# Performance work log

Hardware: AMD Instinct MI355X
Metric: run time of the kernel (lower is better)

## Reference

```python
import jax, jax.numpy as jnp
import numpy as np

B, T, D, H = 2, 1024, 1024, 16
K = D            # key_dim = hidden * expand_k (1.0)
V = 2 * D        # value_dim = hidden * expand_v (2.0)
DK, DV = K // H, V // H
I = 2816         # SwiGLU intermediate
CONV = 4
EPS = 1e-6


def rmsnorm(x, w, eps=EPS):
    return x * jax.lax.rsqrt(jnp.mean(x * x, -1, keepdims=True) + eps) * w


def l2norm(x, eps=EPS):
    return x * jax.lax.rsqrt(jnp.sum(x * x, -1, keepdims=True) + eps)


def short_conv(x, w):
    # depthwise causal conv1d (kernel CONV, no bias) + silu; x [B,T,C], w [C,CONV]
    kern = w.T[:, None, :]  # [CONV, 1, C]
    y = jax.lax.conv_general_dilated(
        x, kern, (1,), [(CONV - 1, 0)],
        dimension_numbers=('NWC', 'WIO', 'NWC'),
        feature_group_count=x.shape[-1])
    return jax.nn.silu(y)


def setup_inputs() -> dict:
    key = jax.random.key(0)
    ks = jax.random.split(key, 20)
    p = lambda i, shape, s=0.02: jax.random.normal(ks[i], shape, jnp.float32) * s
    return dict(
        x=jax.random.normal(ks[0], (B, T, D), jnp.float32),
        norm1_w=jnp.ones((D,), jnp.float32),
        wq=p(1, (D, K)), wk=p(2, (D, K)), wv=p(3, (D, V)),
        conv_q=p(4, (K, CONV), 0.3), conv_k=p(5, (K, CONV), 0.3), conv_v=p(6, (V, CONV), 0.3),
        wb=p(7, (D, H)), wa=p(8, (D, H)),
        A_log=jnp.log(jax.random.uniform(ks[9], (H,), jnp.float32, 1.0, 16.0)),
        dt_bias=jnp.log(jnp.expm1(jax.random.uniform(ks[10], (H,), jnp.float32, 0.001, 0.1))),
        wg=p(11, (D, V)),
        o_norm_w=jnp.ones((DV,), jnp.float32),
        wo=p(12, (V, D)),
        norm2_w=jnp.ones((D,), jnp.float32),
        w1=p(13, (D, I)), w2=p(14, (I, D)), w3=p(15, (D, I)),
    )


def reference(x, norm1_w, wq, wk, wv, conv_q, conv_k, conv_v, wb, wa,
              A_log, dt_bias, wg, o_norm_w, wo, norm2_w, w1, w2, w3):
    h = rmsnorm(x, norm1_w)
    # projections + short causal conv (silu)
    q = short_conv(h @ wq, conv_q).reshape(B, T, H, DK)
    k = short_conv(h @ wk, conv_k).reshape(B, T, H, DK)
    v = short_conv(h @ wv, conv_v).reshape(B, T, H, DV)
    q = l2norm(q) * (DK ** -0.5)
    k = l2norm(k)
    beta = jax.nn.sigmoid(h @ wb)                              # [B,T,H]
    # mamba-style decay gate: g = -exp(A_log) * softplus(a + dt_bias)
    g = -jnp.exp(A_log) * jax.nn.softplus(h @ wa + dt_bias)   # [B,T,H]

    # gated delta rule: S_t = exp(g_t)*S_{t-1}; u_t = beta_t*(v_t - k_t^T S_t);
    # S_t += k_t u_t^T; o_t = q_t^T S_t
    def step(S, inp):
        qt, kt, vt, gt, bt = inp                               # [B,H,*]
        S = S * jnp.exp(gt)[..., None, None]
        u = (vt - jnp.einsum('bhk,bhkv->bhv', kt, S)) * bt[..., None]
        S = S + kt[..., None] * u[:, :, None, :]
        ot = jnp.einsum('bhk,bhkv->bhv', qt, S)
        return S, ot

    S0 = jnp.zeros((B, H, DK, DV), x.dtype)
    seq = (q.transpose(1, 0, 2, 3), k.transpose(1, 0, 2, 3),
           v.transpose(1, 0, 2, 3), g.transpose(1, 0, 2), beta.transpose(1, 0, 2))
    _, o = jax.lax.scan(step, S0, seq)
    o = o.transpose(1, 0, 2, 3)                                # [B,T,H,DV]

    # output gate: per-head RMSNorm * swish(gate), then out-projection
    gate = (h @ wg).reshape(B, T, H, DV)
    o = rmsnorm(o, o_norm_w) * gate * jax.nn.sigmoid(gate)
    x = x + o.reshape(B, T, V) @ wo

    # SwiGLU MLP with residual
    h2 = rmsnorm(x, norm2_w)
    return x + (jax.nn.silu(h2 @ w1) * (h2 @ w3)) @ w2
```

## Files before the change

kernel.cpp:

```cpp
#include <hip/hip_runtime.h>
#include <stdint.h>

typedef unsigned short u16;
typedef float f32x4 __attribute__((ext_vector_type(4)));
typedef __bf16 bf16x8 __attribute__((ext_vector_type(8)));
typedef unsigned short u16x8 __attribute__((ext_vector_type(8)));

#define N1P 6272

__device__ __forceinline__ u16 f2bf(float f) {
    union { float f; uint32_t u; } v; v.f = f;
    uint32_t u = v.u;
    return (u16)((u + 0x7FFFu + ((u >> 16) & 1u)) >> 16);
}
__device__ __forceinline__ float bf2f(u16 h) {
    union { uint32_t u; float f; } v; v.u = ((uint32_t)h) << 16; return v.f;
}
__device__ __forceinline__ float sigm(float x) { return 1.f / (1.f + __expf(-x)); }

__device__ __forceinline__ void async16(const u16* g, u16* l) {
    __builtin_amdgcn_global_load_lds((const __attribute__((address_space(1))) void*)g,
                                     (__attribute__((address_space(3))) void*)l, 16, 0, 0);
}

__device__ __forceinline__ int swz64(int row, int col) {
    return row * 128 + ((((col >> 3) ^ (row & 7)) << 3) + (col & 7)) * 2;
}
__device__ __forceinline__ bf16x8 frag64(const u16* m, int rowbase, int lane, int kk) {
    const int row = rowbase + (lane & 15);
    const int unit = (lane >> 4) + (kk << 2);
    return *(const bf16x8*)((const char*)m + row * 128 + ((unit ^ (row & 7)) << 4));
}

struct TJob { const float* src; u16* dst; int rows, cols, rowOff, rowStride, nOut, blkBase, gx; };
struct TJobs { TJob j[10]; };

__global__ __launch_bounds__(256) void k_transpose_all(TJobs jobs, int njobs) {
    __shared__ float tile[32][33];
    const int bid = blockIdx.x;
    int ji = 0;
#pragma unroll
    for (int i = 1; i < 10; ++i)
        if (i < njobs && bid >= jobs.j[i].blkBase) ji = i;
    const TJob J = jobs.j[ji];
    const int bx = bid - J.blkBase;
    const int n0 = (bx % J.gx) * 32, k0 = (bx / J.gx) * 32;
    const int tx = threadIdx.x, ty = threadIdx.y;
#pragma unroll
    for (int j = 0; j < 32; j += 8) {
        int r = k0 + ty + j, c = n0 + tx;
        tile[ty + j][tx] = (r < J.rows && c < J.cols) ? J.src[(size_t)r * J.cols + c] : 0.f;
    }
    __syncthreads();
#pragma unroll
    for (int j = 0; j < 32; j += 8) {
        int n = n0 + ty + j, k = k0 + tx;
        if (n < J.nOut) J.dst[(size_t)(J.rowOff + n * J.rowStride) * J.rows + k] = f2bf(tile[tx][ty + j]);
    }
}

__global__ __launch_bounds__(256) void k_rmsnorm(const float* __restrict__ x, const float* __restrict__ w,
                                                 u16* __restrict__ out) {
    const int row = blockIdx.x, tid = threadIdx.x, lane = tid & 63, wave = tid >> 6;
    const float4 v = ((const float4*)(x + (size_t)row * 1024))[tid];
    float ss = v.x * v.x + v.y * v.y + v.z * v.z + v.w * v.w;
#pragma unroll
    for (int o = 1; o < 64; o <<= 1) ss += __shfl_xor(ss, o);
    __shared__ float sred[4];
    if (lane == 0) sred[wave] = ss;
    __syncthreads();
    const float tot = sred[0] + sred[1] + sred[2] + sred[3];
    const float rn = rsqrtf(tot * (1.f / 1024.f) + 1e-6f);
    const float4 wv = ((const float4*)w)[tid];
    uint2 pk;
    pk.x = (uint32_t)f2bf(v.x * rn * wv.x) | ((uint32_t)f2bf(v.y * rn * wv.y) << 16);
    pk.y = (uint32_t)f2bf(v.z * rn * wv.z) | ((uint32_t)f2bf(v.w * rn * wv.w) << 16);
    *(uint2*)&out[(size_t)row * 1024 + tid * 4] = pk;
}

template <int TILE, int EPI>
__global__ __launch_bounds__(512) void k_gemm(const u16* __restrict__ A, const u16* __restrict__ Bt,
                                              void* __restrict__ Cout, const float* __restrict__ Res,
                                              int N, int Kd) {
    __shared__ __align__(16) u16 As[2][TILE * 64];
    __shared__ __align__(16) u16 Bs[2][TILE * 64];
    constexpr int MB = 2048 / TILE;
    const int q = (int)gridDim.x >> 3;
    const int bid = blockIdx.x;
    const int wg = (bid & 7) * q + (bid >> 3);
    const int bm = wg & (MB - 1), bn = wg / MB;
    const int tid = threadIdx.x, lane = tid & 63, wave = tid >> 6;
    const int wm = wave >> 2, wn = wave & 3;
    constexpr int RS = TILE / 2, CS = TILE / 4;
    constexpr int FRM = RS / 16, FRN = CS / 16;
    constexpr int IS = TILE / 64;

    const int srow = wave * 8 + (lane >> 3);
    const int scol = ((lane & 7) ^ (lane >> 3)) * 8;
    const u16* gA = A + (size_t)(bm * TILE + srow) * Kd + scol;
    const u16* gB = Bt + (size_t)(bn * TILE + srow) * Kd + scol;

    f32x4 acc[FRM][FRN] = {};
    const int NT = Kd >> 6;

#pragma unroll
    for (int j = 0; j < IS; ++j) {
        async16(gA + (size_t)j * 64 * Kd, &As[0][j * 4096 + wave * 512]);
        async16(gB + (size_t)j * 64 * Kd, &Bs[0][j * 4096 + wave * 512]);
    }
    asm volatile("s_waitcnt vmcnt(0)" ::: "memory");
    __syncthreads();

    int buf = 0;
    for (int t = 0; t < NT; ++t) {
        if (t + 1 < NT) {
            const int k0 = (t + 1) << 6;
#pragma unroll
            for (int j = 0; j < IS; ++j) {
                async16(gA + (size_t)j * 64 * Kd + k0, &As[buf ^ 1][j * 4096 + wave * 512]);
                async16(gB + (size_t)j * 64 * Kd + k0, &Bs[buf ^ 1][j * 4096 + wave * 512]);
            }
        }
#pragma unroll
        for (int kk = 0; kk < 2; ++kk) {
            bf16x8 af[FRM], bfr[FRN];
#pragma unroll
            for (int mi = 0; mi < FRM; ++mi) af[mi] = frag64(As[buf], wm * RS + mi * 16, lane, kk);
#pragma unroll
            for (int ni = 0; ni < FRN; ++ni) bfr[ni] = frag64(Bs[buf], wn * CS + ni * 16, lane, kk);
#pragma unroll
            for (int mi = 0; mi < FRM; ++mi)
#pragma unroll
                for (int ni = 0; ni < FRN; ++ni)
                    acc[mi][ni] = __builtin_amdgcn_mfma_f32_16x16x32_bf16(af[mi], bfr[ni], acc[mi][ni], 0, 0, 0);
        }
        asm volatile("s_waitcnt vmcnt(0)" ::: "memory");
        __syncthreads();
        buf ^= 1;
    }

    const int rsub = (lane >> 4) * 4;
    const int csub = lane & 15;

    if constexpr (EPI == 1) {
        const int crow0 = bm * TILE + wm * RS;
        const int ccol0 = bn * TILE + wn * CS;
#pragma unroll
        for (int mi = 0; mi < FRM; ++mi)
#pragma unroll
            for (int ni = 0; ni < FRN; ++ni) {
                const int c = ccol0 + ni * 16 + csub;
#pragma unroll
                for (int r = 0; r < 4; ++r) {
                    const int rr = crow0 + mi * 16 + rsub + r;
                    ((float*)Cout)[(size_t)rr * N + c] = acc[mi][ni][r] + Res[(size_t)rr * N + c];
                }
            }
    } else if constexpr (EPI == 2) {
        u16* ctile = (u16*)As;
#pragma unroll
        for (int mi = 0; mi < FRM; ++mi)
#pragma unroll
            for (int ni = 0; ni < FRN; ++ni)
#pragma unroll
                for (int r = 0; r < 4; ++r)
                    ctile[(wm * 64 + mi * 16 + rsub + r) * 128 + wn * 32 + ni * 16 + csub] =
                        f2bf(acc[mi][ni][r]);
        __syncthreads();
#pragma unroll
        for (int k = 0; k < 4; ++k) {
            const int f = (tid + k * 512) * 8;
            const int r = f >> 7, c = f & 127;
            *(u16x8*)&((u16*)Cout)[(size_t)(bm * 128 + r) * N + bn * 128 + c] = *(const u16x8*)&ctile[f];
        }
    } else {
        u16* ctile = (u16*)As;
#pragma unroll
        for (int mi = 0; mi < FRM; ++mi)
#pragma unroll
            for (int ni = 0; ni < FRN; ++ni)
#pragma unroll
                for (int r = 0; r < 4; ++r) {
                    const float v = acc[mi][ni][r];
                    const float p = __shfl_xor(v, 1);
                    const float u1 = (lane & 1) ? p : v;
                    const float u3 = (lane & 1) ? v : p;
                    const float res = u1 * sigm(u1) * u3;
                    if (!(lane & 1))
                        ctile[(wm * 64 + mi * 16 + rsub + r) * 64 + ((wn * 32 + ni * 16 + csub) >> 1)] =
                            f2bf(res);
                }
        __syncthreads();
#pragma unroll
        for (int k = 0; k < 2; ++k) {
            const int f = (tid + k * 512) * 8;
            const int r = f >> 6, c = f & 63;
            *(u16x8*)&((u16*)Cout)[(size_t)(bm * 128 + r) * N + bn * 64 + c] = *(const u16x8*)&ctile[f];
        }
    }
}

__global__ __launch_bounds__(256) void k_conv(const u16* __restrict__ P, const float* __restrict__ cwq,
                                              const float* __restrict__ cwk, const float* __restrict__ cwv,
                                              const float* __restrict__ A_log, const float* __restrict__ dtb,
                                              u16* __restrict__ Qb, u16* __restrict__ Kb,
                                              u16* __restrict__ Vb, float* __restrict__ Gl,
                                              float* __restrict__ Bbuf) {
    const int row = blockIdx.x;
    const int t = row & 1023;
    const int tid = threadIdx.x;
    const long prow = (long)row * N1P;
#pragma unroll
    for (int p = 0; p < 2; ++p) {
        const int g = p * 256 + tid;
        const int c = g * 8;
        u16x8 taps[4];
#pragma unroll
        for (int j = 0; j < 4; ++j) {
            const int tt = t - 3 + j;
            if (tt >= 0) taps[j] = *(const u16x8*)&P[prow + (long)(j - 3) * N1P + c];
            else         taps[j] = u16x8{};
        }
        const float* cw = (c < 1024) ? (cwq + c * 4)
                          : (c < 2048) ? (cwk + (c - 1024) * 4)
                                       : (cwv + (c - 2048) * 4);
        float y[8];
#pragma unroll
        for (int e = 0; e < 8; ++e) {
            const float4 w = ((const float4*)cw)[e];
            float v = bf2f(taps[0][e]) * w.x + bf2f(taps[1][e]) * w.y +
                      bf2f(taps[2][e]) * w.z + bf2f(taps[3][e]) * w.w;
            y[e] = v * sigm(v);
        }
        if (c < 2048) {
            float ss = 0.f;
#pragma unroll
            for (int e = 0; e < 8; ++e) ss += y[e] * y[e];
            ss += __shfl_xor(ss, 1); ss += __shfl_xor(ss, 2); ss += __shfl_xor(ss, 4);
            const float rn = rsqrtf(ss + 1e-6f);
            const float sc = (c < 1024) ? rn * 0.125f : rn;
            u16x8 o;
#pragma unroll
            for (int e = 0; e < 8; ++e) o[e] = f2bf(y[e] * sc);
            if (c < 1024) *(u16x8*)&Qb[(size_t)row * 1024 + c] = o;
            else          *(u16x8*)&Kb[(size_t)row * 1024 + (c - 1024)] = o;
        } else {
            u16x8 o;
#pragma unroll
            for (int e = 0; e < 8; ++e) o[e] = f2bf(y[e]);
            *(u16x8*)&Vb[(size_t)row * 2048 + (c - 2048)] = o;
        }
    }
    if (tid < 32) {
        const int h = tid & 15;
        const float val = bf2f(P[prow + 4096 + tid]);
        if (tid < 16) {
            Bbuf[(size_t)row * 16 + h] = sigm(val);
        } else {
            const float a = val + dtb[h];
            const float sp = (a > 15.f) ? a : log1pf(__expf(a));
            Gl[(size_t)row * 16 + h] = -__expf(A_log[h]) * sp;
        }
    }
}

__global__ __launch_bounds__(256) void k_scan1(
    const u16* __restrict__ Qb, const u16* __restrict__ Kb, const u16* __restrict__ Vb,
    const float* __restrict__ Gl, const float* __restrict__ Bb,
    u16* __restrict__ CHW, u16* __restrict__ CHM, u16* __restrict__ CHQc,
    u16* __restrict__ CHKcT, u16* __restrict__ CHU0T, float* __restrict__ CHcC) {
    __shared__ __align__(16) char sm[66048];
    u16* Ql   = (u16*)(sm);
    u16* Kl   = (u16*)(sm + 8192);
    u16* VTb  = (u16*)(sm + 16384);
    u16* KT1b = (u16*)(sm + 32768);
    u16* Mim  = (u16*)(sm + 40960);
    u16* MTim = (u16*)(sm + 49152);
    u16* Tb   = (u16*)(sm + 57344);
    float* Tl    = (float*)sm;
    float* gcs   = (float*)(sm + 65536);
    float* betal = (float*)(sm + 65792);

    const int blk = blockIdx.x;
    const int bb = blk >> 8, h = (blk >> 4) & 15, ch = blk & 15;
    const int bhc = blk;
    const int tid = threadIdx.x, lane = tid & 63, wave = tid >> 6;
    const long rowbase = (long)bb * 1024 + ch * 64;

    if (tid < 64) {
        gcs[tid] = Gl[(rowbase + tid) * 16 + h];
        betal[tid] = Bb[(rowbase + tid) * 16 + h];
    }
    for (int u = tid; u < 512; u += 256) {
        int r = u >> 3, c8 = u & 7;
        uint4 kv = *(const uint4*)&Kb[(rowbase + r) * 1024 + h * 64 + c8 * 8];
        uint4 qv = *(const uint4*)&Qb[(rowbase + r) * 1024 + h * 64 + c8 * 8];
        int b = r * 128 + ((c8 ^ (r & 7)) << 4);
        *(uint4*)((char*)Kl + b) = kv;
        *(uint4*)((char*)Ql + b) = qv;
    }
    __syncthreads();
    if (wave == 0) {
        float g = gcs[lane];
#pragma unroll
        for (int off = 1; off < 64; off <<= 1) {
            float n = __shfl_up(g, off, 64);
            if (lane >= off) g += n;
        }
        gcs[lane] = g;
    }
    for (int u = tid; u < 1024; u += 256) {
        int r = u >> 4, c8 = u & 15;
        u16x8 vv = *(const u16x8*)&Vb[(rowbase + r) * 2048 + h * 128 + c8 * 8];
        float bsc = betal[r];
#pragma unroll
        for (int j = 0; j < 8; ++j) {
            int dv = c8 * 8 + j;
            *(u16*)((char*)VTb + swz64(dv, r)) = f2bf(bf2f(vv[j]) * bsc);
        }
    }
    f32x4 aQK[4] = {}, aKK[4] = {};
#pragma unroll
    for (int nt = 0; nt < 4; ++nt)
#pragma unroll
        for (int kk = 0; kk < 2; ++kk) {
            bf16x8 bq = frag64(Kl, nt * 16, lane, kk);
            aQK[nt] = __builtin_amdgcn_mfma_f32_16x16x32_bf16(frag64(Ql, wave * 16, lane, kk), bq, aQK[nt], 0, 0, 0);
            aKK[nt] = __builtin_amdgcn_mfma_f32_16x16x32_bf16(frag64(Kl, wave * 16, lane, kk), bq, aKK[nt], 0, 0, 0);
        }
    __syncthreads();

    const float gcsC = gcs[63];
    float am[4][4];
#pragma unroll
    for (int nt = 0; nt < 4; ++nt)
#pragma unroll
        for (int reg = 0; reg < 4; ++reg) {
            int t = wave * 16 + ((lane >> 4) << 2) + reg;
            int i = nt * 16 + (lane & 15);
            float dec = __expf(gcs[t] - gcs[i]);
            float mv = (i <= t) ? dec * aQK[nt][reg] : 0.f;
            *(u16*)((char*)CHM + (size_t)bhc * 8192 + swz64(t, i)) = f2bf(mv);
            float a = (i < t) ? betal[t] * dec * aKK[nt][reg] : 0.f;
            am[nt][reg] = -a;
            u16 amb = f2bf(-a);
            *(u16*)((char*)Mim + swz64(t, i)) = amb;
            *(u16*)((char*)MTim + swz64(i, t)) = amb;
        }
    for (int e = tid; e < 4096; e += 256) {
        int r = e >> 6, c = e & 63;
        int ib = swz64(r, c);
        float qv = bf2f(*(const u16*)((const char*)Ql + ib)) * __expf(gcs[r]);
        *(u16*)((char*)CHQc + (size_t)bhc * 8192 + ib) = f2bf(qv);
        float kv = bf2f(*(const u16*)((const char*)Kl + ib));
        int ob = swz64(c, r);
        *(u16*)((char*)KT1b + ob) = f2bf(kv * betal[r] * __expf(gcs[r]));
        *(u16*)((char*)CHKcT + (size_t)bhc * 8192 + ob) = f2bf(kv * __expf(gcsC - gcs[r]));
    }
    if (tid == 0) CHcC[bhc] = __expf(gcsC);
    __syncthreads();

#pragma unroll
    for (int nt = 0; nt < 4; ++nt)
#pragma unroll
        for (int reg = 0; reg < 4; ++reg) {
            int t = wave * 16 + ((lane >> 4) << 2) + reg;
            int i = nt * 16 + (lane & 15);
            float tv = (t == i) ? 1.f : am[nt][reg];
            Tl[t * 64 + i] = tv;
            *(u16*)((char*)Tb + swz64(t, i)) = f2bf(tv);
        }
    __syncthreads();

    const int hi = wave * 16 + 15;
#pragma unroll
    for (int j = 1; j <= 5; ++j) {
        f32x4 aM[4] = {};
#pragma unroll
        for (int nt = 0; nt < 4; ++nt) {
            if (nt * 16 > hi - (1 << j)) continue;
#pragma unroll
            for (int kk = 0; kk < 2; ++kk) {
                if (kk * 32 > hi) break;
                aM[nt] = __builtin_amdgcn_mfma_f32_16x16x32_bf16(
                    frag64(Mim, wave * 16, lane, kk), frag64(MTim, nt * 16, lane, kk), aM[nt], 0, 0, 0);
            }
        }
        __syncthreads();
#pragma unroll
        for (int nt = 0; nt < 4; ++nt)
#pragma unroll
            for (int reg = 0; reg < 4; ++reg) {
                int t = wave * 16 + ((lane >> 4) << 2) + reg;
                int i = nt * 16 + (lane & 15);
                float mv = (t - i >= (1 << j)) ? aM[nt][reg] : 0.f;
                u16 mb = f2bf(mv);
                *(u16*)((char*)Mim + swz64(t, i)) = mb;
                *(u16*)((char*)MTim + swz64(i, t)) = mb;
            }
        __syncthreads();
        f32x4 aT[4];
#pragma unroll
        for (int nt = 0; nt < 4; ++nt)
#pragma unroll
            for (int reg = 0; reg < 4; ++reg) {
                int t = wave * 16 + ((lane >> 4) << 2) + reg;
                int i = nt * 16 + (lane & 15);
                aT[nt][reg] = Tl[t * 64 + i];
            }
#pragma unroll
        for (int nt = 0; nt < 4; ++nt) {
            if (nt * 16 > hi - (1 << j)) continue;
#pragma unroll
            for (int kk = 0; kk < 2; ++kk) {
                if (kk * 32 > hi) break;
                aT[nt] = __builtin_amdgcn_mfma_f32_16x16x32_bf16(
                    frag64(Tb, wave * 16, lane, kk), frag64(MTim, nt * 16, lane, kk), aT[nt], 0, 0, 0);
            }
        }
#pragma unroll
        for (int nt = 0; nt < 4; ++nt)
#pragma unroll
            for (int reg = 0; reg < 4; ++reg) {
                int t = wave * 16 + ((lane >> 4) << 2) + reg;
                int i = nt * 16 + (lane & 15);
                Tl[t * 64 + i] = aT[nt][reg];
                *(u16*)((char*)Tb + swz64(t, i)) = f2bf(aT[nt][reg]);
            }
    }
    __syncthreads();

    {
        f32x4 aW[4] = {};
#pragma unroll
        for (int nt = 0; nt < 4; ++nt)
#pragma unroll
            for (int kk = 0; kk < 2; ++kk) {
                if (kk * 32 > hi) break;
                aW[nt] = __builtin_amdgcn_mfma_f32_16x16x32_bf16(
                    frag64(Tb, wave * 16, lane, kk), frag64(KT1b, nt * 16, lane, kk), aW[nt], 0, 0, 0);
            }
#pragma unroll
        for (int nt = 0; nt < 4; ++nt)
#pragma unroll
            for (int reg = 0; reg < 4; ++reg) {
                int r = wave * 16 + ((lane >> 4) << 2) + reg;
                int c = nt * 16 + (lane & 15);
                *(u16*)((char*)CHW + (size_t)bhc * 8192 + swz64(r, c)) = f2bf(aW[nt][reg]);
            }
    }
#pragma unroll
    for (int rt = 0; rt < 2; ++rt) {
        f32x4 aU[4] = {};
        int rb = (wave * 2 + rt) * 16;
#pragma unroll
        for (int nt = 0; nt < 4; ++nt)
#pragma unroll
            for (int kk = 0; kk < 2; ++kk) {
                if (kk * 32 > nt * 16 + 15) continue;
                aU[nt] = __builtin_amdgcn_mfma_f32_16x16x32_bf16(
                    frag64(VTb, rb, lane, kk), frag64(Tb, nt * 16, lane, kk), aU[nt], 0, 0, 0);
            }
#pragma unroll
        for (int nt = 0; nt < 4; ++nt)
#pragma unroll
            for (int reg = 0; reg < 4; ++reg) {
                int dv = rb + ((lane >> 4) << 2) + reg;
                int c = nt * 16 + (lane & 15);
                *(u16*)((char*)CHU0T + (size_t)bhc * 16384 + swz64(dv, c)) = f2bf(aU[nt][reg]);
            }
    }
}

__global__ __launch_bounds__(256) void k_scan2(
    const u16* __restrict__ CHW, const u16* __restrict__ CHM, const u16* __restrict__ CHQc,
    const u16* __restrict__ CHKcT, const u16* __restrict__ CHU0T, const float* __restrict__ CHcC,
    float* __restrict__ O) {
    __shared__ __align__(16) u16 stg[2][5 * 4096];
    __shared__ __align__(16) u16 STb[4096], uTl[4096];
    __shared__ float ST[64 * 66];
    const int blk = blockIdx.x;
    const int bb = blk >> 5, h = (blk >> 1) & 15, dvh = blk & 1;
    const int bh = bb * 16 + h;
    const int tid = threadIdx.x, lane = tid & 63, wave = tid >> 6;

    for (int e = tid; e < 64 * 66; e += 256) ST[e] = 0.f;
    for (int e = tid; e < 4096; e += 256) STb[e] = 0;

    auto stage = [&](int buf, int ch) {
        const size_t base = (size_t)(bh * 16 + ch);
        const u16* srcs[5] = { CHW + base * 4096, CHM + base * 4096, CHQc + base * 4096,
                               CHKcT + base * 4096, CHU0T + base * 8192 + dvh * 4096 };
#pragma unroll
        for (int s = 0; s < 5; ++s)
#pragma unroll
            for (int r = 0; r < 2; ++r) {
                int ub = r * 256 + wave * 64;
                async16(srcs[s] + (size_t)(ub + lane) * 8, &stg[buf][s * 4096 + ub * 8]);
            }
    };
    stage(0, 0);
    for (int ch = 0; ch < 16; ++ch) {
        const int cur = ch & 1;
        asm volatile("s_waitcnt vmcnt(0)" ::: "memory");
        __syncthreads();
        if (ch < 15) stage(cur ^ 1, ch + 1);
        const u16* sW = &stg[cur][0];
        const u16* sM = &stg[cur][4096];
        const u16* sQc = &stg[cur][8192];
        const u16* sKcT = &stg[cur][12288];
        const u16* sU0 = &stg[cur][16384];
        {
            f32x4 acc[4] = {};
#pragma unroll
            for (int nt = 0; nt < 4; ++nt)
#pragma unroll
                for (int kk = 0; kk < 2; ++kk)
                    acc[nt] = __builtin_amdgcn_mfma_f32_16x16x32_bf16(
                        frag64(STb, wave * 16, lane, kk), frag64(sW, nt * 16, lane, kk), acc[nt], 0, 0, 0);
#pragma unroll
            for (int nt = 0; nt < 4; ++nt)
#pragma unroll
                for (int reg = 0; reg < 4; ++reg) {
                    int dv = wave * 16 + ((lane >> 4) << 2) + reg;
                    int c = nt * 16 + (lane & 15);
                    int b = swz64(dv, c);
                    float u0 = bf2f(*(const u16*)((const char*)sU0 + b));
                    *(u16*)((char*)uTl + b) = f2bf(u0 - acc[nt][reg]);
                }
        }
        __syncthreads();
        f32x4 accO[4] = {}, accS[4] = {};
#pragma unroll
        for (int nt = 0; nt < 4; ++nt)
#pragma unroll
            for (int kk = 0; kk < 2; ++kk) {
                accO[nt] = __builtin_amdgcn_mfma_f32_16x16x32_bf16(
                    frag64(sM, wave * 16, lane, kk), frag64(uTl, nt * 16, lane, kk), accO[nt], 0, 0, 0);
                accO[nt] = __builtin_amdgcn_mfma_f32_16x16x32_bf16(
                    frag64(sQc, wave * 16, lane, kk), frag64(STb, nt * 16, lane, kk), accO[nt], 0, 0, 0);
                accS[nt] = __builtin_amdgcn_mfma_f32_16x16x32_bf16(
                    frag64(uTl, wave * 16, lane, kk), frag64(sKcT, nt * 16, lane, kk), accS[nt], 0, 0, 0);
            }
        __syncthreads();
        const float cC = CHcC[bh * 16 + ch];
#pragma unroll
        for (int nt = 0; nt < 4; ++nt)
#pragma unroll
            for (int reg = 0; reg < 4; ++reg) {
                int rr = wave * 16 + ((lane >> 4) << 2) + reg;
                int cc = nt * 16 + (lane & 15);
                O[((size_t)(bb * 1024 + ch * 64 + rr)) * 2048 + h * 128 + dvh * 64 + cc] = accO[nt][reg];
                float ns = cC * ST[rr * 66 + cc] + accS[nt][reg];
                ST[rr * 66 + cc] = ns;
                *(u16*)((char*)STb + swz64(rr, cc)) = f2bf(ns);
            }
    }
}

__global__ __launch_bounds__(256) void k_gate(const float* __restrict__ O, const u16* __restrict__ P,
                                              const float* __restrict__ onw, u16* __restrict__ OG) {
    const int row = blockIdx.x;
    const int tid = threadIdx.x, lane = tid & 63, wave = tid >> 6;
#pragma unroll
    for (int p = 0; p < 4; ++p) {
        const int h = p * 4 + wave;
        const int dv = lane * 2;
        const float2 o2 = *(const float2*)&O[(size_t)row * 2048 + h * 128 + dv];
        float ss = o2.x * o2.x + o2.y * o2.y;
#pragma unroll
        for (int o = 1; o < 64; o <<= 1) ss += __shfl_xor(ss, o);
        const float rn = rsqrtf(ss * (1.f / 128.f) + 1e-6f);
        const float g0 = bf2f(P[(size_t)row * N1P + 4128 + h * 128 + dv]);
        const float g1 = bf2f(P[(size_t)row * N1P + 4128 + h * 128 + dv + 1]);
        const float r0 = o2.x * rn * onw[dv] * g0 * sigm(g0);
        const float r1 = o2.y * rn * onw[dv + 1] * g1 * sigm(g1);
        const uint32_t pk = (uint32_t)f2bf(r0) | ((uint32_t)f2bf(r1) << 16);
        *(uint32_t*)&OG[(size_t)row * 2048 + h * 128 + dv] = pk;
    }
}

extern "C" void kernel_launch(void* const* d_in, const int* in_sizes, int n_in,
                              void* d_out, int out_size, void* d_ws, size_t ws_size,
                              hipStream_t stream) {
    const float* x   = (const float*)d_in[0];
    const float* n1w = (const float*)d_in[1];
    const float* wq  = (const float*)d_in[2];
    const float* wk  = (const float*)d_in[3];
    const float* wv  = (const float*)d_in[4];
    const float* cq  = (const float*)d_in[5];
    const float* ck  = (const float*)d_in[6];
    const float* cv  = (const float*)d_in[7];
    const float* wb  = (const float*)d_in[8];
    const float* wa  = (const float*)d_in[9];
    const float* Alg = (const float*)d_in[10];
    const float* dtb = (const float*)d_in[11];
    const float* wg  = (const float*)d_in[12];
    const float* onw = (const float*)d_in[13];
    const float* wo  = (const float*)d_in[14];
    const float* n2w = (const float*)d_in[15];
    const float* w1  = (const float*)d_in[16];
    const float* w2  = (const float*)d_in[17];
    const float* w3  = (const float*)d_in[18];

    if (ws_size < 114819072ULL) return;

    char* ws = (char*)d_ws;
    u16*   WcatT = (u16*)(ws + 0);
    u16*   WoT   = (u16*)(ws + 12845056);
    u16*   W13T  = (u16*)(ws + 17039360);
    u16*   W2T   = (u16*)(ws + 28573696);
    u16*   hA    = (u16*)(ws + 34340864);
    u16*   P     = (u16*)(ws + 38535168);
    u16*   Qb    = (u16*)(ws + 64225280);
    u16*   Kb    = (u16*)(ws + 68419584);
    u16*   Vb    = (u16*)(ws + 72613888);
    float* Gl    = (float*)(ws + 81002496);
    float* Bbf   = (float*)(ws + 81133568);
    float* O     = (float*)(ws + 81264640);
    u16*   CHKcT = (u16*)(ws + 98041856);
    u16*   CHU0T = (u16*)(ws + 102236160);
    float* CHcC  = (float*)(ws + 110624768);
    u16*   CHW   = WcatT;
    u16*   CHM   = (u16*)(ws + 4194304);
    u16*   CHQc  = (u16*)(ws + 8388608);
    u16*   Mm  = Qb;
    u16*   OG  = Vb;
    float* X2  = O;
    u16*   h2A = hA;

    TJobs tj;
    tj.j[0] = { wq, WcatT, 1024, 1024,    0, 1, 1024,     0, 32 };
    tj.j[1] = { wk, WcatT, 1024, 1024, 1024, 1, 1024,  1024, 32 };
    tj.j[2] = { wv, WcatT, 1024, 2048, 2048, 1, 2048,  2048, 64 };
    tj.j[3] = { wb, WcatT, 1024,   16, 4096, 1,   16,  4096,  1 };
    tj.j[4] = { wa, WcatT, 1024,   16, 4112, 1,   16,  4128,  1 };
    tj.j[5] = { wg, WcatT, 1024, 2048, 4128, 1, 2144,  4160, 67 };
    tj.j[6] = { wo, WoT,   2048, 1024,    0, 1, 1024,  6304, 32 };
    tj.j[7] = { w1, W13T,  1024, 2816,    0, 2, 2816,  8352, 88 };
    tj.j[8] = { w3, W13T,  1024, 2816,    1, 2, 2816, 11168, 88 };
    tj.j[9] = { w2, W2T,   2816, 1024,    0, 1, 1024, 13984, 32 };
    k_transpose_all<<<16800, dim3(32, 8), 0, stream>>>(tj, 10);

    k_rmsnorm<<<2048, 256, 0, stream>>>(x, n1w, hA);
    k_gemm<128, 2><<<784, 512, 0, stream>>>(hA, WcatT, P, nullptr, N1P, 1024);

    k_conv<<<2048, 256, 0, stream>>>(P, cq, ck, cv, Alg, dtb, Qb, Kb, Vb, Gl, Bbf);

    k_scan1<<<512, 256, 0, stream>>>(Qb, Kb, Vb, Gl, Bbf, CHW, CHM, CHQc, CHKcT, CHU0T, CHcC);
    k_scan2<<<64, 256, 0, stream>>>(CHW, CHM, CHQc, CHKcT, CHU0T, CHcC, O);

    k_gate<<<2048, 256, 0, stream>>>(O, P, onw, OG);
    k_gemm<64, 1><<<512, 512, 0, stream>>>(OG, WoT, X2, x, 1024, 2048);

    k_rmsnorm<<<2048, 256, 0, stream>>>(X2, n2w, h2A);
    k_gemm<128, 3><<<704, 512, 0, stream>>>(h2A, W13T, Mm, nullptr, 2816, 1024);
    k_gemm<64, 1><<<512, 512, 0, stream>>>(Mm, W2T, (float*)d_out, X2, 1024, 2816);
}
```

Measured before the change: 260.8 us.

## Stage GEMM epilogues through padded LDS, block-interleave W1/W3, remap conv rows

The W1/W3 weights are now interleaved in blocks of 16 rows instead of alternating rows. This lets the SwiGLU epilogue pair acc[mi][0] with acc[mi][1] inside one lane, with no cross-lane shuffle and no idle half of the lanes. The residual-add epilogue now goes through a padded float LDS tile, so global stores and residual loads are coalesced float4 accesses instead of scattered scalar ones. The other epilogue tiles get row padding (132/68) to reduce LDS bank conflicts, and the conv kernel remaps block IDs to spread rows across XCDs. In exchange there is an extra LDS round trip and a barrier in the EPI==1 path, plus index math that depends on the new interleaved layout.

```diff
diff --git a/kernel.cpp b/kernel.cpp
--- a/kernel.cpp
+++ b/kernel.cpp
@@ -32,7 +32,7 @@
     return *(const bf16x8*)((const char*)m + row * 128 + ((unit ^ (row & 7)) << 4));
 }
 
-struct TJob { const float* src; u16* dst; int rows, cols, rowOff, rowStride, nOut, blkBase, gx; };
+struct TJob { const float* src; u16* dst; int rows, cols, rowOff, rowStride, nOut, blkBase, gx, mode; };
 struct TJobs { TJob j[10]; };
 
 __global__ __launch_bounds__(256) void k_transpose_all(TJobs jobs, int njobs) {
@@ -55,7 +55,11 @@
 #pragma unroll
     for (int j = 0; j < 32; j += 8) {
         int n = n0 + ty + j, k = k0 + tx;
-        if (n < J.nOut) J.dst[(size_t)(J.rowOff + n * J.rowStride) * J.rows + k] = f2bf(tile[tx][ty + j]);
+        if (n < J.nOut) {
+            int drow = (J.mode == 0) ? (J.rowOff + n * J.rowStride)
+                                     : (J.rowOff + ((n >> 4) << 5) + (n & 15));
+            J.dst[(size_t)drow * J.rows + k] = f2bf(tile[tx][ty + j]);
+        }
     }
 }
 
@@ -82,8 +86,9 @@
 __global__ __launch_bounds__(512) void k_gemm(const u16* __restrict__ A, const u16* __restrict__ Bt,
                                               void* __restrict__ Cout, const float* __restrict__ Res,
                                               int N, int Kd) {
-    __shared__ __align__(16) u16 As[2][TILE * 64];
-    __shared__ __align__(16) u16 Bs[2][TILE * 64];
+    __shared__ __align__(16) char smem[TILE * 512];
+    u16* Asb = (u16*)smem;
+    u16* Bsb = (u16*)(smem + TILE * 256);
     constexpr int MB = 2048 / TILE;
     const int q = (int)gridDim.x >> 3;
     const int bid = blockIdx.x;
@@ -105,8 +110,8 @@
 
 #pragma unroll
     for (int j = 0; j < IS; ++j) {
-        async16(gA + (size_t)j * 64 * Kd, &As[0][j * 4096 + wave * 512]);
-        async16(gB + (size_t)j * 64 * Kd, &Bs[0][j * 4096 + wave * 512]);
+        async16(gA + (size_t)j * 64 * Kd, Asb + j * 4096 + wave * 512);
+        async16(gB + (size_t)j * 64 * Kd, Bsb + j * 4096 + wave * 512);
     }
     asm volatile("s_waitcnt vmcnt(0)" ::: "memory");
     __syncthreads();
@@ -115,19 +120,22 @@
     for (int t = 0; t < NT; ++t) {
         if (t + 1 < NT) {
             const int k0 = (t + 1) << 6;
+            const int bo = (buf ^ 1) * TILE * 64;
 #pragma unroll
             for (int j = 0; j < IS; ++j) {
-                async16(gA + (size_t)j * 64 * Kd + k0, &As[buf ^ 1][j * 4096 + wave * 512]);
-                async16(gB + (size_t)j * 64 * Kd + k0, &Bs[buf ^ 1][j * 4096 + wave * 512]);
-            }
-        }
+                async16(gA + (size_t)j * 64 * Kd + k0, Asb + bo + j * 4096 + wave * 512);
+                async16(gB + (size_t)j * 64 * Kd + k0, Bsb + bo + j * 4096 + wave * 512);
+            }
+        }
+        const u16* Ab = Asb + buf * TILE * 64;
+        const u16* Bb = Bsb + buf * TILE * 64;
 #pragma unroll
         for (int kk = 0; kk < 2; ++kk) {
             bf16x8 af[FRM], bfr[FRN];
 #pragma unroll
-            for (int mi = 0; mi < FRM; ++mi) af[mi] = frag64(As[buf], wm * RS + mi * 16, lane, kk);
-#pragma unroll
-            for (int ni = 0; ni < FRN; ++ni) bfr[ni] = frag64(Bs[buf], wn * CS + ni * 16, lane, kk);
+            for (int mi = 0; mi < FRM; ++mi) af[mi] = frag64(Ab, wm * RS + mi * 16, lane, kk);
+#pragma unroll
+            for (int ni = 0; ni < FRN; ++ni) bfr[ni] = frag64(Bb, wn * CS + ni * 16, lane, kk);
 #pragma unroll
             for (int mi = 0; mi < FRM; ++mi)
 #pragma unroll
@@ -143,59 +151,60 @@
     const int csub = lane & 15;
 
     if constexpr (EPI == 1) {
-        const int crow0 = bm * TILE + wm * RS;
-        const int ccol0 = bn * TILE + wn * CS;
+        float* ctile = (float*)smem;
 #pragma unroll
         for (int mi = 0; mi < FRM; ++mi)
 #pragma unroll
-            for (int ni = 0; ni < FRN; ++ni) {
-                const int c = ccol0 + ni * 16 + csub;
-#pragma unroll
-                for (int r = 0; r < 4; ++r) {
-                    const int rr = crow0 + mi * 16 + rsub + r;
-                    ((float*)Cout)[(size_t)rr * N + c] = acc[mi][ni][r] + Res[(size_t)rr * N + c];
-                }
-            }
+            for (int ni = 0; ni < FRN; ++ni)
+#pragma unroll
+                for (int r = 0; r < 4; ++r)
+                    ctile[(wm * 32 + mi * 16 + rsub + r) * 68 + wn * 16 + ni * 16 + csub] = acc[mi][ni][r];
+        __syncthreads();
+#pragma unroll
+        for (int k = 0; k < 2; ++k) {
+            const int f = (tid + k * 512) * 4;
+            const int r = f >> 6, c = f & 63;
+            float4 v = *(const float4*)&ctile[r * 68 + c];
+            const float4 rv = *(const float4*)&Res[(size_t)(bm * 64 + r) * N + bn * 64 + c];
+            v.x += rv.x; v.y += rv.y; v.z += rv.z; v.w += rv.w;
+            *(float4*)&((float*)Cout)[(size_t)(bm * 64 + r) * N + bn * 64 + c] = v;
+        }
     } else if constexpr (EPI == 2) {
-        u16* ctile = (u16*)As;
+        u16* ctile = (u16*)smem;
 #pragma unroll
         for (int mi = 0; mi < FRM; ++mi)
 #pragma unroll
             for (int ni = 0; ni < FRN; ++ni)
 #pragma unroll
                 for (int r = 0; r < 4; ++r)
-                    ctile[(wm * 64 + mi * 16 + rsub + r) * 128 + wn * 32 + ni * 16 + csub] =
+                    ctile[(wm * 64 + mi * 16 + rsub + r) * 132 + wn * 32 + ni * 16 + csub] =
                         f2bf(acc[mi][ni][r]);
         __syncthreads();
 #pragma unroll
         for (int k = 0; k < 4; ++k) {
             const int f = (tid + k * 512) * 8;
             const int r = f >> 7, c = f & 127;
-            *(u16x8*)&((u16*)Cout)[(size_t)(bm * 128 + r) * N + bn * 128 + c] = *(const u16x8*)&ctile[f];
+            *(u16x8*)&((u16*)Cout)[(size_t)(bm * 128 + r) * N + bn * 128 + c] =
+                *(const u16x8*)&ctile[r * 132 + c];
         }
     } else {
-        u16* ctile = (u16*)As;
+        u16* ctile = (u16*)smem;
 #pragma unroll
         for (int mi = 0; mi < FRM; ++mi)
 #pragma unroll
-            for (int ni = 0; ni < FRN; ++ni)
-#pragma unroll
-                for (int r = 0; r < 4; ++r) {
-                    const float v = acc[mi][ni][r];
-                    const float p = __shfl_xor(v, 1);
-                    const float u1 = (lane & 1) ? p : v;
-                    const float u3 = (lane & 1) ? v : p;
-                    const float res = u1 * sigm(u1) * u3;
-                    if (!(lane & 1))
-                        ctile[(wm * 64 + mi * 16 + rsub + r) * 64 + ((wn * 32 + ni * 16 + csub) >> 1)] =
-                            f2bf(res);
-                }
+            for (int r = 0; r < 4; ++r) {
+                const float u1 = acc[mi][0][r];
+                const float u3 = acc[mi][1][r];
+                ctile[(wm * 64 + mi * 16 + rsub + r) * 68 + wn * 16 + csub] =
+                    f2bf(u1 * sigm(u1) * u3);
+            }
         __syncthreads();
 #pragma unroll
         for (int k = 0; k < 2; ++k) {
             const int f = (tid + k * 512) * 8;
             const int r = f >> 6, c = f & 63;
-            *(u16x8*)&((u16*)Cout)[(size_t)(bm * 128 + r) * N + bn * 64 + c] = *(const u16x8*)&ctile[f];
+            *(u16x8*)&((u16*)Cout)[(size_t)(bm * 128 + r) * N + bn * 64 + c] =
+                *(const u16x8*)&ctile[r * 68 + c];
         }
     }
 }
@@ -206,7 +215,8 @@
                                               u16* __restrict__ Qb, u16* __restrict__ Kb,
                                               u16* __restrict__ Vb, float* __restrict__ Gl,
                                               float* __restrict__ Bbuf) {
-    const int row = blockIdx.x;
+    const int bid = blockIdx.x;
+    const int row = (bid & 7) * 256 + (bid >> 3);
     const int t = row & 1023;
     const int tid = threadIdx.x;
     const long prow = (long)row * N1P;
@@ -630,16 +640,16 @@
     u16*   h2A = hA;
 
     TJobs tj;
-    tj.j[0] = { wq, WcatT, 1024, 1024,    0, 1, 1024,     0, 32 };
-    tj.j[1] = { wk, WcatT, 1024, 1024, 1024, 1, 1024,  1024, 32 };
-    tj.j[2] = { wv, WcatT, 1024, 2048, 2048, 1, 2048,  2048, 64 };
-    tj.j[3] = { wb, WcatT, 1024,   16, 4096, 1,   16,  4096,  1 };
-    tj.j[4] = { wa, WcatT, 1024,   16, 4112, 1,   16,  4128,  1 };
-    tj.j[5] = { wg, WcatT, 1024, 2048, 4128, 1, 2144,  4160, 67 };
-    tj.j[6] = { wo, WoT,   2048, 1024,    0, 1, 1024,  6304, 32 };
-    tj.j[7] = { w1, W13T,  1024, 2816,    0, 2, 2816,  8352, 88 };
-    tj.j[8] = { w3, W13T,  1024, 2816,    1, 2, 2816, 11168, 88 };
-    tj.j[9] = { w2, W2T,   2816, 1024,    0, 1, 1024, 13984, 32 };
+    tj.j[0] = { wq, WcatT, 1024, 1024,    0, 1, 1024,     0, 32, 0 };
+    tj.j[1] = { wk, WcatT, 1024, 1024, 1024, 1, 1024,  1024, 32, 0 };
+    tj.j[2] = { wv, WcatT, 1024, 2048, 2048, 1, 2048,  2048, 64, 0 };
+    tj.j[3] = { wb, WcatT, 1024,   16, 4096, 1,   16,  4096,  1, 0 };
+    tj.j[4] = { wa, WcatT, 1024,   16, 4112, 1,   16,  4128,  1, 0 };
+    tj.j[5] = { wg, WcatT, 1024, 2048, 4128, 1, 2144,  4160, 67, 0 };
+    tj.j[6] = { wo, WoT,   2048, 1024,    0, 1, 1024,  6304, 32, 0 };
+    tj.j[7] = { w1, W13T,  1024, 2816,    0, 1, 2816,  8352, 88, 1 };
+    tj.j[8] = { w3, W13T,  1024, 2816,   16, 1, 2816, 11168, 88, 1 };
+    tj.j[9] = { w2, W2T,   2816, 1024,    0, 1, 1024, 13984, 32, 0 };
     k_transpose_all<<<16800, dim3(32, 8), 0, stream>>>(tj, 10);
 
     k_rmsnorm<<<2048, 256, 0, stream>>>(x, n1w, hA);
```

Measured after the change: 247.5 us. -5.1%, faster.
